# Kernel optimization log

Measured on AMD Instinct MI355X. Metric: run time of the kernel, lower is better.

## Reference

```python
import jax, jax.numpy as jnp
import numpy as np

N = 8192       # num_nodes
F_IN = 128     # num_features
H = 32         # hidden_dim
C = 10         # num_classes
E = 262144     # num_edges (avg degree 32)
EPS = 1e-5     # BatchNorm1d eps


def setup_inputs() -> dict:
    key = jax.random.key(0)
    ks = jax.random.split(key, 24)
    rn = lambda k, shape, s=0.05: jax.random.normal(k, shape, jnp.float32) * s
    z = lambda n: jnp.zeros((n,), jnp.float32)
    return {
        "b": jax.random.normal(ks[0], (N, N), jnp.float32),
        "x": jax.random.normal(ks[1], (N, F_IN), jnp.float32),
        "edge_index": jax.random.randint(ks[2], (2, E), 0, N, jnp.int32),
        # GCNConv weights (stored [in,out]) + biases
        "W0": rn(ks[3], (F_IN, H)), "bc0": z(H),
        "W1": rn(ks[4], (H, H)),    "bc1": z(H),
        # BatchNorm affine params
        "g0": jnp.ones((H,), jnp.float32), "be0": z(H),
        "g1": jnp.ones((H,), jnp.float32), "be1": z(H),
        # autoencoder Linears (stored [in,out])
        "Wa0": rn(ks[5], (N, H)), "ba0": z(H),
        "Wa1": rn(ks[6], (H, H)), "ba1": z(H),
        "Wa2": rn(ks[7], (H, H)), "ba2": z(H),
        "Wa3": rn(ks[8], (H, N)), "ba3": z(N),
        # jump classifier: Linear(num_layers*H, C)
        "Wj": rn(ks[9], (2 * H, C)), "bj": z(C),
    }


def _gcn_conv(x, W, bias, src, dst):
    # PyG GCNConv: D^{-1/2}(A+I)D^{-1/2} X W + bias (src/dst already include self-loops)
    h = x @ W                                             # [N, out]
    deg = jax.ops.segment_sum(jnp.ones(src.shape[0], h.dtype), dst, num_segments=N)
    dinv = jax.lax.rsqrt(deg)                             # deg >= 1 due to self-loops
    norm = dinv[src] * dinv[dst]                          # [E+N]
    agg = jax.ops.segment_sum(norm[:, None] * h[src], dst, num_segments=N)
    return agg + bias


def _bn(x, g, b):
    # BatchNorm1d in training mode: batch stats over node dim, biased variance
    m = jnp.mean(x, axis=0)
    v = jnp.var(x, axis=0)
    return g * (x - m) * jax.lax.rsqrt(v + EPS) + b


def reference(b, x, edge_index, W0, bc0, W1, bc1, g0, be0, g1, be1,
              Wa0, ba0, Wa1, ba1, Wa2, ba2, Wa3, ba3, Wj, bj):
    loop = jnp.arange(N, dtype=edge_index.dtype)
    src = jnp.concatenate([edge_index[0], loop])
    dst = jnp.concatenate([edge_index[1], loop])

    # layer 0
    h = jax.nn.relu(_bn(_gcn_conv(x, W0, bc0, src, dst), g0, be0))
    x0 = h
    b = b @ Wa0 + ba0          # [N, H]
    h = h + b
    # layer 1
    h = jax.nn.relu(_bn(_gcn_conv(h, W1, bc1, src, dst), g1, be1))
    x1 = h
    b = b @ Wa1 + ba1
    # (torch computes x = x1 + b here, but it is dead after the last layer)
    # decoder tail: autoencoder[2], autoencoder[3]
    b = b @ Wa2 + ba2
    b = b @ Wa3 + ba3          # [N, N]

    out = jnp.concatenate([x0, x1], axis=1) @ Wj + bj
    return jax.nn.log_softmax(out, axis=-1), b
```

## Files before the change

kernel.cpp:

```cpp
#include <hip/hip_runtime.h>
#include <math.h>

#define NN 8192
#define FIN 128
#define HD 32
#define NC 10
#define NE 262144
#define EPSBN 1e-5f

typedef short short8 __attribute__((ext_vector_type(8)));
typedef float f32x4 __attribute__((ext_vector_type(4)));
typedef unsigned short us4 __attribute__((ext_vector_type(4)));

__device__ __forceinline__ float bf2f(unsigned short b) {
  unsigned int u = ((unsigned int)b) << 16;
  float f;
  __builtin_memcpy(&f, &u, 4);
  return f;
}
__device__ __forceinline__ unsigned short f2bf(float f) {
  unsigned int u;
  __builtin_memcpy(&u, &f, 4);
  u = u + 0x7fffu + ((u >> 16) & 1u);
  return (unsigned short)(u >> 16);
}
__device__ __forceinline__ short8 ld_bf8(const unsigned short* p) {
  uint4 u = *(const uint4*)p;
  return __builtin_bit_cast(short8, u);
}
__device__ __forceinline__ float ldin(const void* p, int i, int isf) {
  if (isf) return ((const float*)p)[i];
  return bf2f(((const unsigned short*)p)[i]);
}

__global__ void detect_k(const void* __restrict__ b, int* __restrict__ flag,
                         float* __restrict__ stats, int* __restrict__ dz) {
  const unsigned short* p = (const unsigned short*)b;
  int t = threadIdx.x;
  unsigned short s = p[2 * t];
  int e = (s >> 7) & 0xFF;
  int hit = (e >= 110 && e <= 135) ? 1 : 0;
  __shared__ int cnt[256];
  cnt[t] = hit;
  stats[t] = 0.0f;
  for (int i = t; i < 2 * NN; i += 256) dz[i] = 0;
  __syncthreads();
  for (int o = 128; o > 0; o >>= 1) {
    if (t < o) cnt[t] += cnt[t + o];
    __syncthreads();
  }
  if (t == 0) flag[0] = (cnt[0] < 128) ? 1 : 0;
}

__global__ void compute_Rp(const void* __restrict__ Wa1, const void* __restrict__ ba1,
                           const void* __restrict__ Wa2, const void* __restrict__ ba2,
                           const void* __restrict__ Wa3, const void* __restrict__ ba3,
                           const int* __restrict__ flg,
                           float* __restrict__ r2, unsigned short* __restrict__ Rp) {
  int isf = *flg;
  __shared__ float sW1[1024], sW2[1024], sT[1024], sv[32];
  int t = threadIdx.x;
  for (int i = t; i < 1024; i += 256) {
    sW1[i] = ldin(Wa1, i, isf);
    sW2[i] = ldin(Wa2, i, isf);
  }
  __syncthreads();
  for (int i = t; i < 1024; i += 256) {
    int c = i >> 5, c2 = i & 31;
    float acc = 0.f;
    for (int k = 0; k < 32; k++) acc += sW1[c * 32 + k] * sW2[k * 32 + c2];
    sT[i] = acc;
  }
  if (t < 32) {
    float acc = ldin(ba2, t, isf);
    for (int k = 0; k < 32; k++) acc += ldin(ba1, k, isf) * sW2[k * 32 + t];
    sv[t] = acc;
  }
  __syncthreads();
  int j = blockIdx.x * 256 + t;
  float w3[32];
  for (int c = 0; c < 32; c++) w3[c] = ldin(Wa3, c * NN + j, isf);
  float rr = ldin(ba3, j, isf);
  for (int c = 0; c < 32; c++) rr += sv[c] * w3[c];
  r2[j] = rr;
  float Rcol[32];
  for (int c = 0; c < 32; c++) {
    float acc = 0.f;
    for (int cp = 0; cp < 32; cp++) acc += sT[c * 32 + cp] * w3[cp];
    Rcol[c] = acc;
  }
  int jt = j >> 4, n = j & 15;
  for (int q = 0; q < 4; q++)
    for (int jj = 0; jj < 8; jj++)
      Rp[(size_t)(jt * 64 + q * 16 + n) * 8 + jj] = f2bf(Rcol[q * 8 + jj]);
}

__global__ void pack_Bp(const void* __restrict__ Wa0, const int* __restrict__ flg,
                        unsigned short* __restrict__ Bp) {
  int isf = *flg;
  int tid = blockIdx.x * 256 + threadIdx.x;
  int kb = tid >> 7;
  int h = (tid >> 6) & 1;
  int L = tid & 63;
  int q = L >> 4, n = L & 15;
  int base_k = kb * 32 + q * 8;
  if (isf) {
    const float* W = (const float*)Wa0;
    for (int j = 0; j < 8; j++)
      Bp[(size_t)((kb * 2 + h) * 64 + L) * 8 + j] = f2bf(W[(base_k + j) * HD + h * 16 + n]);
  } else {
    const unsigned short* W = (const unsigned short*)Wa0;
    for (int j = 0; j < 8; j++)
      Bp[(size_t)((kb * 2 + h) * 64 + L) * 8 + j] = W[(base_k + j) * HD + h * 16 + n];
  }
}

__global__ void deg_k(const int* __restrict__ dst, int* __restrict__ deg) {
  int e = blockIdx.x * 256 + threadIdx.x;
  atomicAdd(&deg[dst[e]], 1);
}

__global__ void csr_scan(const int* __restrict__ deg, int* __restrict__ rowp,
                         float* __restrict__ dinvf) {
  __shared__ int ps[1024];
  int t = threadIdx.x;
  int base = t * 8;
  int loc[8];
  int s = 0;
  for (int j = 0; j < 8; j++) {
    int d = deg[base + j];
    loc[j] = s;
    s += d;
    dinvf[base + j] = rsqrtf((float)d + 1.0f);
  }
  ps[t] = s;
  __syncthreads();
  for (int off = 1; off < 1024; off <<= 1) {
    int v = (t >= off) ? ps[t - off] : 0;
    __syncthreads();
    if (t >= off) ps[t] += v;
    __syncthreads();
  }
  int ex = (t > 0) ? ps[t - 1] : 0;
  for (int j = 0; j < 8; j++) rowp[base + j] = ex + loc[j];
  if (t == 1023) rowp[NN] = ex + s;
}

__global__ void csr_fill(const int* __restrict__ src, const int* __restrict__ dst,
                         const int* __restrict__ rowp, int* __restrict__ cnt,
                         int* __restrict__ col) {
  int e = blockIdx.x * 256 + threadIdx.x;
  int d = dst[e];
  int pos = atomicAdd(&cnt[d], 1);
  col[rowp[d] + pos] = src[e];
}

__global__ void gemm_x_w0(const void* __restrict__ x, const void* __restrict__ W0,
                          const float* __restrict__ dinvf, const int* __restrict__ flg,
                          float* __restrict__ h0) {
  int isf = *flg;
  __shared__ float sW[FIN * HD];
  __shared__ float sx[8 * FIN];
  int t = threadIdx.x;
  for (int i = t; i < FIN * HD; i += 256) sW[i] = ldin(W0, i, isf);
  int row0 = blockIdx.x * 8;
  for (int i = t; i < 8 * FIN; i += 256) {
    int r = i >> 7, k = i & 127;
    sx[i] = ldin(x, (row0 + r) * FIN + k, isf);
  }
  __syncthreads();
  int r = t >> 5, c = t & 31;
  float acc = 0.f;
  for (int k = 0; k < FIN; k++) acc += sx[r * FIN + k] * sW[k * HD + c];
  h0[(row0 + r) * HD + c] = acc * dinvf[row0 + r];
}

__global__ void gather_agg(const int* __restrict__ rowp, const int* __restrict__ col,
                           const float* __restrict__ dinvf, const float* __restrict__ hs,
                           float* __restrict__ agg) {
  int w = (blockIdx.x << 2) + (threadIdx.x >> 6);
  int L = threadIdx.x & 63;
  int c = L & 31, half = L >> 5;
  int s0 = rowp[w], s1 = rowp[w + 1];
  float acc = 0.f;
  int e = s0 + half;
  if (e < s1) {
    int s = col[e];
    for (e += 2; e < s1; e += 2) {
      int sn = col[e];
      acc += hs[(size_t)s * HD + c];
      s = sn;
    }
    acc += hs[(size_t)s * HD + c];
  }
  acc += __shfl_xor(acc, 32);
  if (half == 0) {
    float tot = acc + hs[(size_t)w * HD + c];
    agg[(size_t)w * HD + c] = dinvf[w] * tot;
  }
}

__global__ void bn_stats(const float* __restrict__ xin, float* __restrict__ sum, float* __restrict__ sq) {
  int t = threadIdx.x;
  int c = t & 31;
  int g = t >> 5;
  float s = 0.f, q = 0.f;
  for (int r = blockIdx.x * 8 + g; r < NN; r += 2048) {
    float v = xin[r * HD + c];
    s += v;
    q += v * v;
  }
  __shared__ float ss[256], qq[256];
  ss[t] = s; qq[t] = q;
  __syncthreads();
  if (t < 128) { ss[t] += ss[t + 128]; qq[t] += qq[t + 128]; }
  __syncthreads();
  if (t < 64) { ss[t] += ss[t + 64]; qq[t] += qq[t + 64]; }
  __syncthreads();
  if (t < 32) {
    atomicAdd(&sum[c], ss[t] + ss[t + 32]);
    atomicAdd(&sq[c], qq[t] + qq[t + 32]);
  }
}

__global__ void fuse0_w1(float* __restrict__ aggA, const float* __restrict__ b1,
                         const void* __restrict__ ba0, const void* __restrict__ W1,
                         const float* __restrict__ sum0, const float* __restrict__ sq0,
                         const void* __restrict__ g0, const void* __restrict__ be0,
                         const float* __restrict__ dinvf, const int* __restrict__ flg,
                         float* __restrict__ x0) {
  int isf = *flg;
  __shared__ float sW[1024], sh[16 * 33];
  int t = threadIdx.x;
  for (int i = t; i < 1024; i += 512) sW[i] = ldin(W1, i, isf);
  int r = t >> 5, c = t & 31;
  int row = blockIdx.x * 16 + r;
  float m = sum0[c] * (1.0f / 8192.0f);
  float var = fmaxf(sq0[c] * (1.0f / 8192.0f) - m * m, 0.0f);
  float ac = ldin(g0, c, isf) * rsqrtf(var + EPSBN);
  float bc = ldin(be0, c, isf) - m * ac;
  float v = aggA[row * HD + c];
  float xv = fmaxf(ac * v + bc, 0.0f);
  x0[row * HD + c] = xv;
  sh[r * 33 + c] = xv + b1[row * HD + c] + ldin(ba0, c, isf);
  __syncthreads();
  float acc = 0.f;
  for (int k = 0; k < 32; k++) acc += sh[r * 33 + k] * sW[k * HD + c];
  aggA[row * HD + c] = acc * dinvf[row];
}

__global__ void gemm_b_wa0(const void* __restrict__ Bm, const unsigned short* __restrict__ Bp,
                           const int* __restrict__ flg, float* __restrict__ b1) {
  int isf = *flg;
  __shared__ float red[8][512];
  int t = threadIdx.x;
  int kq = t >> 6;
  int L = t & 63;
  int rt = blockIdx.x;
  int q = L >> 4, n = L & 15;
  size_t aoff = (size_t)(rt * 16 + n) * NN + kq * 1024 + q * 8;
  f32x4 acc0 = {0.f, 0.f, 0.f, 0.f};
  f32x4 acc1 = {0.f, 0.f, 0.f, 0.f};
  int kb0 = kq * 32;
  if (isf) {
    const float* arow = (const float*)Bm + aoff;
    for (int i = 0; i < 32; i++) {
      f32x4 u0 = *(const f32x4*)(arow + i * 32);
      f32x4 u1 = *(const f32x4*)(arow + i * 32 + 4);
      union { unsigned short s[8]; short8 v; } au;
      au.s[0] = f2bf(u0[0]); au.s[1] = f2bf(u0[1]); au.s[2] = f2bf(u0[2]); au.s[3] = f2bf(u0[3]);
      au.s[4] = f2bf(u1[0]); au.s[5] = f2bf(u1[1]); au.s[6] = f2bf(u1[2]); au.s[7] = f2bf(u1[3]);
      const unsigned short* bpp = Bp + (size_t)((kb0 + i) * 2) * 512 + L * 8;
      acc0 = __builtin_amdgcn_mfma_f32_16x16x32_bf16(au.v, ld_bf8(bpp), acc0, 0, 0, 0);
      acc1 = __builtin_amdgcn_mfma_f32_16x16x32_bf16(au.v, ld_bf8(bpp + 512), acc1, 0, 0, 0);
    }
  } else {
    const unsigned short* arow = (const unsigned short*)Bm + aoff;
    for (int i = 0; i < 32; i++) {
      short8 a = ld_bf8(arow + i * 32);
      const unsigned short* bpp = Bp + (size_t)((kb0 + i) * 2) * 512 + L * 8;
      acc0 = __builtin_amdgcn_mfma_f32_16x16x32_bf16(a, ld_bf8(bpp), acc0, 0, 0, 0);
      acc1 = __builtin_amdgcn_mfma_f32_16x16x32_bf16(a, ld_bf8(bpp + 512), acc1, 0, 0, 0);
    }
  }
  for (int r = 0; r < 4; r++) {
    red[kq][(q * 4 + r) * 32 + n] = acc0[r];
    red[kq][(q * 4 + r) * 32 + n + 16] = acc1[r];
  }
  __syncthreads();
  float s = 0.f;
  for (int kw = 0; kw < 8; kw++) s += red[kw][t];
  b1[rt * 512 + t] = s;
}

__global__ void classifier(const float* __restrict__ x0, const float* __restrict__ agg1,
                           const float* __restrict__ sum1, const float* __restrict__ sq1,
                           const void* __restrict__ g1, const void* __restrict__ be1,
                           const void* __restrict__ Wj, const void* __restrict__ bj,
                           const int* __restrict__ flg, void* __restrict__ outv) {
  int isf = *flg;
  __shared__ float sW[64 * NC];
  __shared__ float sb[NC];
  __shared__ float sa[HD], sbb[HD];
  __shared__ float sx0[64 * 33], sx1[64 * 33];
  int t = threadIdx.x;
  for (int i = t; i < 64 * NC; i += 64) sW[i] = ldin(Wj, i, isf);
  if (t < NC) sb[t] = ldin(bj, t, isf);
  if (t < HD) {
    float m = sum1[t] * (1.0f / 8192.0f);
    float var = fmaxf(sq1[t] * (1.0f / 8192.0f) - m * m, 0.0f);
    float ac = ldin(g1, t, isf) * rsqrtf(var + EPSBN);
    sa[t] = ac;
    sbb[t] = ldin(be1, t, isf) - m * ac;
  }
  int row0 = blockIdx.x * 64;
  for (int i = t; i < 64 * HD; i += 64) {
    int r = i >> 5, k = i & 31;
    sx0[r * 33 + k] = x0[(size_t)row0 * HD + i];
    sx1[r * 33 + k] = agg1[(size_t)row0 * HD + i];
  }
  __syncthreads();
  float lg[NC];
  for (int c = 0; c < NC; c++) lg[c] = sb[c];
  for (int k = 0; k < HD; k++) {
    float v = sx0[t * 33 + k];
    for (int c = 0; c < NC; c++) lg[c] += v * sW[k * NC + c];
  }
  for (int k = 0; k < HD; k++) {
    float v = fmaxf(sa[k] * sx1[t * 33 + k] + sbb[k], 0.0f);
    for (int c = 0; c < NC; c++) lg[c] += v * sW[(HD + k) * NC + c];
  }
  float mx = lg[0];
  for (int c = 1; c < NC; c++) mx = fmaxf(mx, lg[c]);
  float se = 0.f;
  for (int c = 0; c < NC; c++) se += expf(lg[c] - mx);
  float lse = mx + logf(se);
  int row = row0 + t;
  if (isf) {
    float* o = (float*)outv;
    for (int c = 0; c < NC; c++) o[row * NC + c] = lg[c] - lse;
  } else {
    unsigned short* o = (unsigned short*)outv;
    for (int c = 0; c < NC; c++) o[row * NC + c] = f2bf(lg[c] - lse);
  }
}

__global__ void gemm_b4(const float* __restrict__ b1, const void* __restrict__ ba0,
                        const unsigned short* __restrict__ Rp, const float* __restrict__ r2,
                        const int* __restrict__ flg, void* __restrict__ outv) {
  int isf = *flg;
  int t = threadIdx.x;
  int w = (blockIdx.x << 2) + (t >> 6);
  int L = t & 63;
  int rt = w >> 3, jc = w & 7;
  int q = L >> 4, n = L & 15;
  const float* ap = b1 + (size_t)(rt * 16 + n) * HD + q * 8;
  union { unsigned short s[8]; short8 v; } au;
  for (int j = 0; j < 8; j++) au.s[j] = f2bf(ap[j] + ldin(ba0, q * 8 + j, isf));
  short8 bfrag = au.v;
  int orow = rt * 16 + n;
  float* of = (float*)outv + NN * NC;
  unsigned short* ob = (unsigned short*)outv + NN * NC;
  for (int jt = jc * 64; jt < (jc + 1) * 64; jt++) {
    short8 afrag = ld_bf8(Rp + (size_t)(jt * 64 + L) * 8);
    f32x4 acc = {0.f, 0.f, 0.f, 0.f};
    acc = __builtin_amdgcn_mfma_f32_16x16x32_bf16(afrag, bfrag, acc, 0, 0, 0);
    int col = jt * 16 + q * 4;
    f32x4 radd = *(const f32x4*)(r2 + col);
    f32x4 res = acc + radd;
    size_t base = (size_t)orow * NN + col;
    if (isf) {
      *(f32x4*)(of + base) = res;
    } else {
      us4 pk;
      pk[0] = f2bf(res[0]); pk[1] = f2bf(res[1]); pk[2] = f2bf(res[2]); pk[3] = f2bf(res[3]);
      *(us4*)(ob + base) = pk;
    }
  }
}

extern "C" void kernel_launch(void* const* d_in, const int* in_sizes, int n_in,
                              void* d_out, int out_size, void* d_ws, size_t ws_size,
                              hipStream_t stream) {
  const void* B   = d_in[0];
  const void* X   = d_in[1];
  const int* EI   = (const int*)d_in[2];
  const void* W0  = d_in[3];
  const void* W1  = d_in[5];
  const void* g0  = d_in[7];
  const void* be0 = d_in[8];
  const void* g1  = d_in[9];
  const void* be1 = d_in[10];
  const void* Wa0 = d_in[11];
  const void* ba0 = d_in[12];
  const void* Wa1 = d_in[13];
  const void* ba1 = d_in[14];
  const void* Wa2 = d_in[15];
  const void* ba2 = d_in[16];
  const void* Wa3 = d_in[17];
  const void* ba3 = d_in[18];
  const void* Wj  = d_in[19];
  const void* bj  = d_in[20];
  (void)in_sizes; (void)n_in; (void)ws_size;

  const int* esrc = EI;
  const int* edst = EI + NE;

  float* ws   = (float*)d_ws;
  int* flag   = (int*)ws;
  float* stats = ws + 16;
  float* sum0 = stats, * sq0 = stats + 32, * sum1 = stats + 64, * sq1 = stats + 96;
  float* b1   = stats + 256;
  float* r2   = b1 + NN * HD;
  unsigned short* Rp = (unsigned short*)(r2 + NN);

  size_t outBytesMin = (size_t)out_size * 2;
  size_t scratchBytes = (size_t)(NN + 3 * NN * HD) * 4
                      + (size_t)(256 * 2 * 64 * 8) * 2
                      + (size_t)(3 * NN + 1 + NE) * 4;
  char* sc = (char*)d_out + ((outBytesMin - scratchBytes) & ~(size_t)255);
  float* degf = (float*)sc;
  float* aggA = degf + NN;
  float* aggB = aggA + NN * HD;
  float* x0h  = aggB + NN * HD;
  unsigned short* Bp = (unsigned short*)(x0h + NN * HD);
  int* deg_i  = (int*)(Bp + 256 * 2 * 64 * 8);
  int* cnt    = deg_i + NN;
  int* rowp   = cnt + NN;
  int* col    = rowp + NN + 1;

  detect_k<<<1, 256, 0, stream>>>(B, flag, stats, deg_i);
  compute_Rp<<<32, 256, 0, stream>>>(Wa1, ba1, Wa2, ba2, Wa3, ba3, flag, r2, Rp);
  pack_Bp<<<128, 256, 0, stream>>>(Wa0, flag, Bp);
  deg_k<<<NE / 256, 256, 0, stream>>>(edst, deg_i);
  csr_scan<<<1, 1024, 0, stream>>>(deg_i, rowp, degf);
  csr_fill<<<NE / 256, 256, 0, stream>>>(esrc, edst, rowp, cnt, col);
  gemm_x_w0<<<NN / 8, 256, 0, stream>>>(X, W0, degf, flag, x0h);
  gemm_b_wa0<<<512, 512, 0, stream>>>(B, Bp, flag, b1);
  gather_agg<<<NN / 4, 256, 0, stream>>>(rowp, col, degf, x0h, aggA);
  bn_stats<<<256, 256, 0, stream>>>(aggA, sum0, sq0);
  fuse0_w1<<<NN / 16, 512, 0, stream>>>(aggA, b1, ba0, W1, sum0, sq0, g0, be0,
                                        degf, flag, x0h);
  gather_agg<<<NN / 4, 256, 0, stream>>>(rowp, col, degf, aggA, aggB);
  bn_stats<<<256, 256, 0, stream>>>(aggB, sum1, sq1);
  classifier<<<NN / 64, 64, 0, stream>>>(x0h, aggB, sum1, sq1, g1, be1, Wj, bj, flag, d_out);
  gemm_b4<<<1024, 256, 0, stream>>>(b1, ba0, Rp, r2, flag, d_out);
}
```

Before: 748.0 us.

## Merge small prep kernels and fuse BatchNorm statistics into gather aggregation

Several small launches are merged into one grid split by block ranges: detection, Rp and Bp packing and degree counting go into prep_all, and CSR fill is combined with the x@W0 GEMM. The dtype flag kernel is dropped, and each kernel now works out the input dtype itself with a wave ballot. BatchNorm sum and sum-of-squares are accumulated inside the gather kernel through shared-memory and sharded global atomics, which removes the separate bn_stats passes. The aim is to cut launch count, serial dependencies and a re-read of the aggregates, in exchange for more atomics and redundant per-block detection.

```diff
diff --git a/kernel.cpp b/kernel.cpp
--- a/kernel.cpp
+++ b/kernel.cpp
@@ -33,33 +33,49 @@
   return bf2f(((const unsigned short*)p)[i]);
 }
 
-__global__ void detect_k(const void* __restrict__ b, int* __restrict__ flag,
-                         float* __restrict__ stats, int* __restrict__ dz) {
+__device__ __forceinline__ int wave_detect(const void* b) {
   const unsigned short* p = (const unsigned short*)b;
-  int t = threadIdx.x;
-  unsigned short s = p[2 * t];
+  int lane = threadIdx.x & 63;
+  unsigned short s = p[2 * lane];
   int e = (s >> 7) & 0xFF;
-  int hit = (e >= 110 && e <= 135) ? 1 : 0;
-  __shared__ int cnt[256];
-  cnt[t] = hit;
-  stats[t] = 0.0f;
-  for (int i = t; i < 2 * NN; i += 256) dz[i] = 0;
-  __syncthreads();
-  for (int o = 128; o > 0; o >>= 1) {
-    if (t < o) cnt[t] += cnt[t + o];
-    __syncthreads();
-  }
-  if (t == 0) flag[0] = (cnt[0] < 128) ? 1 : 0;
-}
-
-__global__ void compute_Rp(const void* __restrict__ Wa1, const void* __restrict__ ba1,
-                           const void* __restrict__ Wa2, const void* __restrict__ ba2,
-                           const void* __restrict__ Wa3, const void* __restrict__ ba3,
-                           const int* __restrict__ flg,
-                           float* __restrict__ r2, unsigned short* __restrict__ Rp) {
-  int isf = *flg;
+  unsigned long long m = __ballot(e >= 110 && e <= 135);
+  return (__popcll(m) < 33) ? 1 : 0;
+}
+
+__global__ void prep_all(const void* __restrict__ B,
+                         const void* __restrict__ Wa1, const void* __restrict__ ba1,
+                         const void* __restrict__ Wa2, const void* __restrict__ ba2,
+                         const void* __restrict__ Wa3, const void* __restrict__ ba3,
+                         const void* __restrict__ Wa0, const int* __restrict__ edst,
+                         int* __restrict__ deg, float* __restrict__ r2,
+                         unsigned short* __restrict__ Rp, unsigned short* __restrict__ Bp) {
+  int bid = blockIdx.x;
+  int t = threadIdx.x;
+  if (bid >= 160) {
+    int e = (bid - 160) * 256 + t;
+    atomicAdd(&deg[edst[e]], 1);
+    return;
+  }
+  int isf = wave_detect(B);
+  if (bid >= 32) {
+    int tid = (bid - 32) * 256 + t;
+    int kb = tid >> 7;
+    int h = (tid >> 6) & 1;
+    int L = tid & 63;
+    int q = L >> 4, n = L & 15;
+    int base_k = kb * 32 + q * 8;
+    if (isf) {
+      const float* W = (const float*)Wa0;
+      for (int j = 0; j < 8; j++)
+        Bp[(size_t)((kb * 2 + h) * 64 + L) * 8 + j] = f2bf(W[(base_k + j) * HD + h * 16 + n]);
+    } else {
+      const unsigned short* W = (const unsigned short*)Wa0;
+      for (int j = 0; j < 8; j++)
+        Bp[(size_t)((kb * 2 + h) * 64 + L) * 8 + j] = W[(base_k + j) * HD + h * 16 + n];
+    }
+    return;
+  }
   __shared__ float sW1[1024], sW2[1024], sT[1024], sv[32];
-  int t = threadIdx.x;
   for (int i = t; i < 1024; i += 256) {
     sW1[i] = ldin(Wa1, i, isf);
     sW2[i] = ldin(Wa2, i, isf);
@@ -77,7 +93,7 @@
     sv[t] = acc;
   }
   __syncthreads();
-  int j = blockIdx.x * 256 + t;
+  int j = bid * 256 + t;
   float w3[32];
   for (int c = 0; c < 32; c++) w3[c] = ldin(Wa3, c * NN + j, isf);
   float rr = ldin(ba3, j, isf);
@@ -95,35 +111,11 @@
       Rp[(size_t)(jt * 64 + q * 16 + n) * 8 + jj] = f2bf(Rcol[q * 8 + jj]);
 }
 
-__global__ void pack_Bp(const void* __restrict__ Wa0, const int* __restrict__ flg,
-                        unsigned short* __restrict__ Bp) {
-  int isf = *flg;
-  int tid = blockIdx.x * 256 + threadIdx.x;
-  int kb = tid >> 7;
-  int h = (tid >> 6) & 1;
-  int L = tid & 63;
-  int q = L >> 4, n = L & 15;
-  int base_k = kb * 32 + q * 8;
-  if (isf) {
-    const float* W = (const float*)Wa0;
-    for (int j = 0; j < 8; j++)
-      Bp[(size_t)((kb * 2 + h) * 64 + L) * 8 + j] = f2bf(W[(base_k + j) * HD + h * 16 + n]);
-  } else {
-    const unsigned short* W = (const unsigned short*)Wa0;
-    for (int j = 0; j < 8; j++)
-      Bp[(size_t)((kb * 2 + h) * 64 + L) * 8 + j] = W[(base_k + j) * HD + h * 16 + n];
-  }
-}
-
-__global__ void deg_k(const int* __restrict__ dst, int* __restrict__ deg) {
-  int e = blockIdx.x * 256 + threadIdx.x;
-  atomicAdd(&deg[dst[e]], 1);
-}
-
 __global__ void csr_scan(const int* __restrict__ deg, int* __restrict__ rowp,
-                         float* __restrict__ dinvf) {
+                         float* __restrict__ dinvf, float* __restrict__ stats) {
   __shared__ int ps[1024];
   int t = threadIdx.x;
+  if (t < 512) stats[t] = 0.0f;
   int base = t * 8;
   int loc[8];
   int s = 0;
@@ -146,27 +138,27 @@
   if (t == 1023) rowp[NN] = ex + s;
 }
 
-__global__ void csr_fill(const int* __restrict__ src, const int* __restrict__ dst,
+__global__ void fill_xw0(const int* __restrict__ esrc, const int* __restrict__ edst,
                          const int* __restrict__ rowp, int* __restrict__ cnt,
-                         int* __restrict__ col) {
-  int e = blockIdx.x * 256 + threadIdx.x;
-  int d = dst[e];
-  int pos = atomicAdd(&cnt[d], 1);
-  col[rowp[d] + pos] = src[e];
-}
-
-__global__ void gemm_x_w0(const void* __restrict__ x, const void* __restrict__ W0,
-                          const float* __restrict__ dinvf, const int* __restrict__ flg,
-                          float* __restrict__ h0) {
-  int isf = *flg;
+                         int* __restrict__ col, const void* __restrict__ X,
+                         const void* __restrict__ W0, const float* __restrict__ dinvf,
+                         const void* __restrict__ B, float* __restrict__ h0) {
+  int bid = blockIdx.x, t = threadIdx.x;
+  if (bid < 1024) {
+    int e = bid * 256 + t;
+    int d = edst[e];
+    int pos = atomicAdd(&cnt[d], 1);
+    col[rowp[d] + pos] = esrc[e];
+    return;
+  }
+  int isf = wave_detect(B);
   __shared__ float sW[FIN * HD];
   __shared__ float sx[8 * FIN];
-  int t = threadIdx.x;
   for (int i = t; i < FIN * HD; i += 256) sW[i] = ldin(W0, i, isf);
-  int row0 = blockIdx.x * 8;
+  int row0 = (bid - 1024) * 8;
   for (int i = t; i < 8 * FIN; i += 256) {
     int r = i >> 7, k = i & 127;
-    sx[i] = ldin(x, (row0 + r) * FIN + k, isf);
+    sx[i] = ldin(X, (row0 + r) * FIN + k, isf);
   }
   __syncthreads();
   int r = t >> 5, c = t & 31;
@@ -175,83 +167,9 @@
   h0[(row0 + r) * HD + c] = acc * dinvf[row0 + r];
 }
 
-__global__ void gather_agg(const int* __restrict__ rowp, const int* __restrict__ col,
-                           const float* __restrict__ dinvf, const float* __restrict__ hs,
-                           float* __restrict__ agg) {
-  int w = (blockIdx.x << 2) + (threadIdx.x >> 6);
-  int L = threadIdx.x & 63;
-  int c = L & 31, half = L >> 5;
-  int s0 = rowp[w], s1 = rowp[w + 1];
-  float acc = 0.f;
-  int e = s0 + half;
-  if (e < s1) {
-    int s = col[e];
-    for (e += 2; e < s1; e += 2) {
-      int sn = col[e];
-      acc += hs[(size_t)s * HD + c];
-      s = sn;
-    }
-    acc += hs[(size_t)s * HD + c];
-  }
-  acc += __shfl_xor(acc, 32);
-  if (half == 0) {
-    float tot = acc + hs[(size_t)w * HD + c];
-    agg[(size_t)w * HD + c] = dinvf[w] * tot;
-  }
-}
-
-__global__ void bn_stats(const float* __restrict__ xin, float* __restrict__ sum, float* __restrict__ sq) {
-  int t = threadIdx.x;
-  int c = t & 31;
-  int g = t >> 5;
-  float s = 0.f, q = 0.f;
-  for (int r = blockIdx.x * 8 + g; r < NN; r += 2048) {
-    float v = xin[r * HD + c];
-    s += v;
-    q += v * v;
-  }
-  __shared__ float ss[256], qq[256];
-  ss[t] = s; qq[t] = q;
-  __syncthreads();
-  if (t < 128) { ss[t] += ss[t + 128]; qq[t] += qq[t + 128]; }
-  __syncthreads();
-  if (t < 64) { ss[t] += ss[t + 64]; qq[t] += qq[t + 64]; }
-  __syncthreads();
-  if (t < 32) {
-    atomicAdd(&sum[c], ss[t] + ss[t + 32]);
-    atomicAdd(&sq[c], qq[t] + qq[t + 32]);
-  }
-}
-
-__global__ void fuse0_w1(float* __restrict__ aggA, const float* __restrict__ b1,
-                         const void* __restrict__ ba0, const void* __restrict__ W1,
-                         const float* __restrict__ sum0, const float* __restrict__ sq0,
-                         const void* __restrict__ g0, const void* __restrict__ be0,
-                         const float* __restrict__ dinvf, const int* __restrict__ flg,
-                         float* __restrict__ x0) {
-  int isf = *flg;
-  __shared__ float sW[1024], sh[16 * 33];
-  int t = threadIdx.x;
-  for (int i = t; i < 1024; i += 512) sW[i] = ldin(W1, i, isf);
-  int r = t >> 5, c = t & 31;
-  int row = blockIdx.x * 16 + r;
-  float m = sum0[c] * (1.0f / 8192.0f);
-  float var = fmaxf(sq0[c] * (1.0f / 8192.0f) - m * m, 0.0f);
-  float ac = ldin(g0, c, isf) * rsqrtf(var + EPSBN);
-  float bc = ldin(be0, c, isf) - m * ac;
-  float v = aggA[row * HD + c];
-  float xv = fmaxf(ac * v + bc, 0.0f);
-  x0[row * HD + c] = xv;
-  sh[r * 33 + c] = xv + b1[row * HD + c] + ldin(ba0, c, isf);
-  __syncthreads();
-  float acc = 0.f;
-  for (int k = 0; k < 32; k++) acc += sh[r * 33 + k] * sW[k * HD + c];
-  aggA[row * HD + c] = acc * dinvf[row];
-}
-
 __global__ void gemm_b_wa0(const void* __restrict__ Bm, const unsigned short* __restrict__ Bp,
-                           const int* __restrict__ flg, float* __restrict__ b1) {
-  int isf = *flg;
+                           float* __restrict__ b1) {
+  int isf = wave_detect(Bm);
   __shared__ float red[8][512];
   int t = threadIdx.x;
   int kq = t >> 6;
@@ -293,12 +211,76 @@
   b1[rt * 512 + t] = s;
 }
 
+__global__ void gather_bn(const int* __restrict__ rowp, const int* __restrict__ col,
+                          const float* __restrict__ dinvf, const float* __restrict__ hs,
+                          float* __restrict__ agg, float* __restrict__ sums) {
+  __shared__ float bs[32], bq[32];
+  int t = threadIdx.x;
+  if (t < 32) { bs[t] = 0.f; bq[t] = 0.f; }
+  __syncthreads();
+  int w = (blockIdx.x << 2) + (t >> 6);
+  int L = t & 63;
+  int c = L & 31, half = L >> 5;
+  int s0 = rowp[w], s1 = rowp[w + 1];
+  float a0 = 0.f, a1 = 0.f;
+  int e = s0 + half;
+  for (; e + 2 < s1; e += 4) {
+    int sA = col[e];
+    int sB = col[e + 2];
+    a0 += hs[sA * HD + c];
+    a1 += hs[sB * HD + c];
+  }
+  if (e < s1) a0 += hs[col[e] * HD + c];
+  float acc = a0 + a1;
+  acc += __shfl_xor(acc, 32);
+  if (half == 0) {
+    float v = dinvf[w] * (acc + hs[w * HD + c]);
+    agg[w * HD + c] = v;
+    atomicAdd(&bs[c], v);
+    atomicAdd(&bq[c], v * v);
+  }
+  __syncthreads();
+  if (t < 32) {
+    int sh = blockIdx.x & 3;
+    atomicAdd(&sums[sh * 32 + t], bs[t]);
+    atomicAdd(&sums[128 + sh * 32 + t], bq[t]);
+  }
+}
+
+__global__ void fuse0_w1(float* __restrict__ aggA, const float* __restrict__ b1,
+                         const void* __restrict__ ba0, const void* __restrict__ W1,
+                         const float* __restrict__ st0,
+                         const void* __restrict__ g0, const void* __restrict__ be0,
+                         const float* __restrict__ dinvf, const void* __restrict__ B,
+                         float* __restrict__ x0) {
+  int isf = wave_detect(B);
+  __shared__ float sW[1024], sh[16 * 33];
+  int t = threadIdx.x;
+  for (int i = t; i < 1024; i += 512) sW[i] = ldin(W1, i, isf);
+  int r = t >> 5, c = t & 31;
+  int row = blockIdx.x * 16 + r;
+  float ssum = st0[c] + st0[32 + c] + st0[64 + c] + st0[96 + c];
+  float ssq = st0[128 + c] + st0[160 + c] + st0[192 + c] + st0[224 + c];
+  float m = ssum * (1.0f / 8192.0f);
+  float var = fmaxf(ssq * (1.0f / 8192.0f) - m * m, 0.0f);
+  float ac = ldin(g0, c, isf) * rsqrtf(var + EPSBN);
+  float bc = ldin(be0, c, isf) - m * ac;
+  float v = aggA[row * HD + c];
+  float xv = fmaxf(ac * v + bc, 0.0f);
+  x0[row * HD + c] = xv;
+  sh[r * 33 + c] = xv + b1[row * HD + c] + ldin(ba0, c, isf);
+  __syncthreads();
+  float acc = 0.f;
+  for (int k = 0; k < 32; k++) acc += sh[r * 33 + k] * sW[k * HD + c];
+  aggA[row * HD + c] = acc * dinvf[row];
+}
+
 __global__ void classifier(const float* __restrict__ x0, const float* __restrict__ agg1,
-                           const float* __restrict__ sum1, const float* __restrict__ sq1,
+                           const float* __restrict__ st1,
                            const void* __restrict__ g1, const void* __restrict__ be1,
                            const void* __restrict__ Wj, const void* __restrict__ bj,
-                           const int* __restrict__ flg, void* __restrict__ outv) {
-  int isf = *flg;
+                           const void* __restrict__ B, void* __restrict__ outv) {
+  int isf = wave_detect(B);
   __shared__ float sW[64 * NC];
   __shared__ float sb[NC];
   __shared__ float sa[HD], sbb[HD];
@@ -307,8 +289,10 @@
   for (int i = t; i < 64 * NC; i += 64) sW[i] = ldin(Wj, i, isf);
   if (t < NC) sb[t] = ldin(bj, t, isf);
   if (t < HD) {
-    float m = sum1[t] * (1.0f / 8192.0f);
-    float var = fmaxf(sq1[t] * (1.0f / 8192.0f) - m * m, 0.0f);
+    float ssum = st1[t] + st1[32 + t] + st1[64 + t] + st1[96 + t];
+    float ssq = st1[128 + t] + st1[160 + t] + st1[192 + t] + st1[224 + t];
+    float m = ssum * (1.0f / 8192.0f);
+    float var = fmaxf(ssq * (1.0f / 8192.0f) - m * m, 0.0f);
     float ac = ldin(g1, t, isf) * rsqrtf(var + EPSBN);
     sa[t] = ac;
     sbb[t] = ldin(be1, t, isf) - m * ac;
@@ -347,8 +331,8 @@
 
 __global__ void gemm_b4(const float* __restrict__ b1, const void* __restrict__ ba0,
                         const unsigned short* __restrict__ Rp, const float* __restrict__ r2,
-                        const int* __restrict__ flg, void* __restrict__ outv) {
-  int isf = *flg;
+                        const void* __restrict__ B, void* __restrict__ outv) {
+  int isf = wave_detect(B);
   int t = threadIdx.x;
   int w = (blockIdx.x << 2) + (t >> 6);
   int L = t & 63;
@@ -406,12 +390,12 @@
   const int* esrc = EI;
   const int* edst = EI + NE;
 
-  float* ws   = (float*)d_ws;
-  int* flag   = (int*)ws;
-  float* stats = ws + 16;
-  float* sum0 = stats, * sq0 = stats + 32, * sum1 = stats + 64, * sq1 = stats + 96;
-  float* b1   = stats + 256;
-  float* r2   = b1 + NN * HD;
+  float* ws    = (float*)d_ws;
+  float* stats = ws;
+  float* st0   = stats;
+  float* st1   = stats + 256;
+  float* b1    = stats + 512;
+  float* r2    = b1 + NN * HD;
   unsigned short* Rp = (unsigned short*)(r2 + NN);
 
   size_t outBytesMin = (size_t)out_size * 2;
@@ -429,20 +413,16 @@
   int* rowp   = cnt + NN;
   int* col    = rowp + NN + 1;
 
-  detect_k<<<1, 256, 0, stream>>>(B, flag, stats, deg_i);
-  compute_Rp<<<32, 256, 0, stream>>>(Wa1, ba1, Wa2, ba2, Wa3, ba3, flag, r2, Rp);
-  pack_Bp<<<128, 256, 0, stream>>>(Wa0, flag, Bp);
-  deg_k<<<NE / 256, 256, 0, stream>>>(edst, deg_i);
-  csr_scan<<<1, 1024, 0, stream>>>(deg_i, rowp, degf);
-  csr_fill<<<NE / 256, 256, 0, stream>>>(esrc, edst, rowp, cnt, col);
-  gemm_x_w0<<<NN / 8, 256, 0, stream>>>(X, W0, degf, flag, x0h);
-  gemm_b_wa0<<<512, 512, 0, stream>>>(B, Bp, flag, b1);
-  gather_agg<<<NN / 4, 256, 0, stream>>>(rowp, col, degf, x0h, aggA);
-  bn_stats<<<256, 256, 0, stream>>>(aggA, sum0, sq0);
-  fuse0_w1<<<NN / 16, 512, 0, stream>>>(aggA, b1, ba0, W1, sum0, sq0, g0, be0,
-                                        degf, flag, x0h);
-  gather_agg<<<NN / 4, 256, 0, stream>>>(rowp, col, degf, aggA, aggB);
-  bn_stats<<<256, 256, 0, stream>>>(aggB, sum1, sq1);
-  classifier<<<NN / 64, 64, 0, stream>>>(x0h, aggB, sum1, sq1, g1, be1, Wj, bj, flag, d_out);
-  gemm_b4<<<1024, 256, 0, stream>>>(b1, ba0, Rp, r2, flag, d_out);
-}
+  hipMemsetAsync(deg_i, 0, (size_t)2 * NN * sizeof(int), stream);
+  prep_all<<<1184, 256, 0, stream>>>(B, Wa1, ba1, Wa2, ba2, Wa3, ba3, Wa0,
+                                     edst, deg_i, r2, Rp, Bp);
+  csr_scan<<<1, 1024, 0, stream>>>(deg_i, rowp, degf, stats);
+  fill_xw0<<<2048, 256, 0, stream>>>(esrc, edst, rowp, cnt, col, X, W0, degf, B, x0h);
+  gemm_b_wa0<<<512, 512, 0, stream>>>(B, Bp, b1);
+  gather_bn<<<NN / 4, 256, 0, stream>>>(rowp, col, degf, x0h, aggA, st0);
+  fuse0_w1<<<NN / 16, 512, 0, stream>>>(aggA, b1, ba0, W1, st0, g0, be0,
+                                        degf, B, x0h);
+  gather_bn<<<NN / 4, 256, 0, stream>>>(rowp, col, degf, aggA, aggB, st1);
+  classifier<<<NN / 64, 64, 0, stream>>>(x0h, aggB, st1, g1, be1, Wj, bj, B, d_out);
+  gemm_b4<<<1024, 256, 0, stream>>>(b1, ba0, Rp, r2, B, d_out);
+}
```

Measured after the change: 746.0 us. About the same (-0.3%).
